# Optimization experiments

Hardware: AMD Instinct MI355X
Metric: run time of the kernel (lower is better)

The kernel has to match this reference:

```python
import jax, jax.numpy as jnp
import numpy as np

N_GAUSS = 512
PLANE = 512


def setup_inputs() -> dict:
    key = jax.random.key(0)
    k1, k2, k3, k4, k5 = jax.random.split(key, 5)
    mean = jax.random.uniform(k1, (N_GAUSS, 2, 1), dtype=jnp.float32)
    alpha = jax.random.uniform(k2, (N_GAUSS, 1), dtype=jnp.float32)
    scale = jax.random.uniform(k3, (N_GAUSS, 2), dtype=jnp.float32)
    theta = jax.random.uniform(k4, (N_GAUSS, 1), dtype=jnp.float32)
    rgb = jax.random.uniform(k5, (N_GAUSS, 3), dtype=jnp.float32)
    # render plane: torch.meshgrid(x, y, indexing='xy'), stack([x, y], -1)
    lin = jnp.linspace(0.0, 1.0, PLANE, dtype=jnp.float32)
    xx, yy = jnp.meshgrid(lin, lin, indexing='xy')
    pixels = jnp.stack([xx, yy], axis=-1)  # (H, W, 2)
    return {"mean": mean, "alpha": alpha, "scale": scale, "theta": theta,
            "rgb": rgb, "pixels": pixels}


def _forward(mean, alpha, scale, theta, rgb, pixels):
    two_pi = 2.0 * jnp.pi
    # covariance = R S S^T R^T with R from circular_activation(theta)
    ta = two_pi * theta                      # (N,1)
    c = jnp.cos(ta)
    s = jnp.sin(ta)
    rot = jnp.stack([jnp.concatenate([c, -s], axis=-1),
                     jnp.concatenate([s, c], axis=-1)], axis=-2)   # (N,2,2)
    smat = jnp.eye(2, dtype=scale.dtype)[None] * scale[..., None]  # (N,2,2)
    cov = rot @ smat @ jnp.swapaxes(smat, -1, -2) @ jnp.swapaxes(rot, -1, -2)
    a = cov[:, 0, 0]
    b01 = cov[:, 0, 1]
    b10 = cov[:, 1, 0]
    d = cov[:, 1, 1]
    det = a * d - b01 * b10                  # (N,)
    inv00 = d / det
    inv01 = -b01 / det
    inv10 = -b10 / det
    inv11 = a / det
    # quadratic form per pixel (analytic 2x2, same math as diff^T inv diff)
    mu = mean[:, :, 0]                       # (N,2)
    dx = pixels[None, :, :, 0] - mu[:, 0][:, None, None]  # (N,H,W)
    dy = pixels[None, :, :, 1] - mu[:, 1][:, None, None]  # (N,H,W)
    q = (inv00[:, None, None] * dx * dx
         + (inv01 + inv10)[:, None, None] * dx * dy
         + inv11[:, None, None] * dy * dy)
    prob = jnp.exp(-0.5 * q) / (two_pi * jnp.sqrt(det))[:, None, None]  # (N,H,W)
    splat = prob / jnp.max(prob)             # global max-normalize
    weighted = rgb * alpha                   # (N,3) rgb * alpha mask
    img = jnp.einsum('nhw,nc->hwc', splat, weighted)  # sum over gaussians
    return jax.nn.sigmoid(img)               # (H,W,3)


def reference(mean, alpha, scale, theta, rgb, pixels):
    return _forward(mean, alpha, scale, theta, rgb, pixels)
```

## Files before the change

### kernel.cpp

```cpp
#include <hip/hip_runtime.h>

#define NG 512
#define PLANE 512

typedef float v2f __attribute__((ext_vector_type(2)));

#define PRM_OFF  16
#define SLOT_OFF 4352

__global__ __launch_bounds__(256) void prep_kernel(
    const float* __restrict__ mean, const float* __restrict__ alpha,
    const float* __restrict__ scale, const float* __restrict__ theta,
    const float* __restrict__ rgb, float* __restrict__ ws) {
    const int n   = blockIdx.x;
    const int tid = threadIdx.x;

    const float TWO_PI = 6.283185307179586f;
    float th = theta[n];
    float c = __builtin_amdgcn_cosf(th);
    float s = __builtin_amdgcn_sinf(th);
    float sx = scale[2 * n], sy = scale[2 * n + 1];

    float m200 = (c * sx) * sx;
    float m201 = (-(s * sy)) * sy;
    float m210 = (s * sx) * sx;
    float m211 = (c * sy) * sy;
    float a   = m200 * c + m201 * (-s);
    float b01 = m200 * s + m201 * c;
    float b10 = m210 * c + m211 * (-s);
    float d   = m210 * s + m211 * c;

    float det = a * d - b01 * b10;
    float rdet = __builtin_amdgcn_rcpf(det);
    float inv00 = d * rdet;
    float inv01 = -b01 * rdet;
    float inv10 = -b10 * rdet;
    float inv11 = a * rdet;

    float norm = __builtin_amdgcn_rcpf(TWO_PI * __builtin_amdgcn_sqrtf(det));
    const float K = -0.5f * 1.4426950408889634f;

    float A_ = K * inv00;
    float B_ = K * (inv01 + inv10);
    float C_ = K * inv11;
    float mx = mean[2 * n], my = mean[2 * n + 1];
    float Lg = fmaf(-0.5f, __builtin_amdgcn_logf(det), -2.651496129472319f);

    if (tid == 0) {
        float w = alpha[n] * norm;
        float4* p = (float4*)(ws + PRM_OFF + 8 * n);
        p[0] = make_float4(A_, B_, C_, mx);
        p[1] = make_float4(my, w * rgb[3 * n], w * rgb[3 * n + 1], w * rgb[3 * n + 2]);
    }

    const float STEP = 1.0f / 511.0f;
    float inv2A = __builtin_amdgcn_rcpf(2.0f * A_);
    float t = -1e30f;
#pragma unroll
    for (int k = 0; k < 2; ++k) {
        int r = tid + (k << 8);
        float y  = (float)r * STEP;
        float dy = y - my;
        float bdy  = B_ * dy;
        float cdy2 = C_ * (dy * dy);
        float xstar = mx - bdy * inv2A;
        float xs = fminf(fmaxf(xstar, 0.0f), 1.0f);
        int i1 = min((int)(xs * 511.0f), 510);
#pragma unroll
        for (int kk = -1; kk <= 2; ++kk) {
            int i = max(0, min(i1 + kk, 511));
            float x = (float)i * STEP;
            float dx = x - mx;
            float q = fmaf(fmaf(A_, dx, bdy), dx, cdy2);
            t = fmaxf(t, q);
        }
    }
    t += Lg;

#pragma unroll
    for (int off = 32; off > 0; off >>= 1)
        t = fmaxf(t, __shfl_xor(t, off));
    __shared__ float sm[4];
    if ((tid & 63) == 0) sm[tid >> 6] = t;
    __syncthreads();
    if (tid == 0) {
        float mm = fmaxf(fmaxf(sm[0], sm[1]), fmaxf(sm[2], sm[3]));
        ws[SLOT_OFF + n] = mm;
    }
}

__global__ __launch_bounds__(512, 4) void splat_kernel(
    const float* __restrict__ pixels, const float* __restrict__ ws,
    float* __restrict__ out) {
    const int tid  = threadIdx.x;
    const int wv   = __builtin_amdgcn_readfirstlane(tid >> 6);
    const int lane = tid & 63;
    const int quad = blockIdx.x * 64 + lane;
    const int pbase = quad << 2;
    const int row  = blockIdx.x >> 1;

    __shared__ float4 shbuf[1536];

    {
        const float4* p = reinterpret_cast<const float4*>(ws + PRM_OFF) + 2 * tid;
        float4 p0 = p[0];
        float4 p1 = p[1];
        float yb = pixels[(row << 10) + 1];
        float dy   = yb - p1.x;
        float bdy  = p0.y * dy;
        float cdy2 = p0.z * (dy * dy);
        shbuf[2 * tid]     = make_float4(p0.x, p0.w, bdy, cdy2);
        shbuf[2 * tid + 1] = make_float4(p1.y, p1.z, p1.w, 0.f);
    }
    __syncthreads();

    float4 p01 = *reinterpret_cast<const float4*>(pixels + 2 * pbase);
    float4 p23 = *reinterpret_cast<const float4*>(pixels + 2 * pbase + 4);
    const v2f x01 = {p01.x, p01.z};
    const v2f x23 = {p23.x, p23.z};

    v2f ar01 = {0.f, 0.f}, ag01 = {0.f, 0.f}, ab01 = {0.f, 0.f};
    v2f ar23 = {0.f, 0.f}, ag23 = {0.f, 0.f}, ab23 = {0.f, 0.f};

    const float4* chunk = shbuf + (wv << 7);
#pragma unroll 8
    for (int n = 0; n < 64; ++n) {
        float4 ta = chunk[2 * n];
        float4 tb = chunk[2 * n + 1];

        float A_ = ta.x, mx = ta.y, bdy = ta.z, cdy2 = ta.w;
        v2f Av = {A_, A_}, mxv = {mx, mx}, bdyv = {bdy, bdy}, cdv = {cdy2, cdy2};

        v2f dx01 = x01 - mxv;
        v2f dx23 = x23 - mxv;
        v2f t01 = __builtin_elementwise_fma(Av, dx01, bdyv);
        v2f t23 = __builtin_elementwise_fma(Av, dx23, bdyv);
        v2f q01 = __builtin_elementwise_fma(t01, dx01, cdv);
        v2f q23 = __builtin_elementwise_fma(t23, dx23, cdv);

        v2f e01 = {__builtin_amdgcn_exp2f(q01.x), __builtin_amdgcn_exp2f(q01.y)};
        v2f e23 = {__builtin_amdgcn_exp2f(q23.x), __builtin_amdgcn_exp2f(q23.y)};

        v2f wrv = {tb.x, tb.x}, wgv = {tb.y, tb.y}, wbv = {tb.z, tb.z};
        ar01 = __builtin_elementwise_fma(e01, wrv, ar01);
        ag01 = __builtin_elementwise_fma(e01, wgv, ag01);
        ab01 = __builtin_elementwise_fma(e01, wbv, ab01);
        ar23 = __builtin_elementwise_fma(e23, wrv, ar23);
        ag23 = __builtin_elementwise_fma(e23, wgv, ag23);
        ab23 = __builtin_elementwise_fma(e23, wbv, ab23);
    }

    float invmax;
    {
        const float4* sl = reinterpret_cast<const float4*>(ws + SLOT_OFF) + 2 * lane;
        float4 s0 = sl[0], s1 = sl[1];
        float m = fmaxf(fmaxf(fmaxf(s0.x, s0.y), fmaxf(s0.z, s0.w)),
                        fmaxf(fmaxf(s1.x, s1.y), fmaxf(s1.z, s1.w)));
#pragma unroll
        for (int off = 32; off > 0; off >>= 1)
            m = fmaxf(m, __shfl_xor(m, off));
        invmax = __builtin_amdgcn_exp2f(-m);
    }

    __syncthreads();

    {
        const int base = ((wv << 6) + lane) * 3;
        shbuf[base + 0] = make_float4(ar01.x, ag01.x, ab01.x, ar01.y);
        shbuf[base + 1] = make_float4(ag01.y, ab01.y, ar23.x, ag23.x);
        shbuf[base + 2] = make_float4(ab23.x, ar23.y, ag23.y, ab23.y);
    }
    __syncthreads();

    if (tid < 192) {
        const int l    = tid / 3;
        const int slot = tid - 3 * l;
        float4 v = shbuf[l * 3 + slot];
#pragma unroll
        for (int cch = 1; cch < 8; ++cch) {
            float4 u = shbuf[((cch << 6) + l) * 3 + slot];
            v.x += u.x; v.y += u.y; v.z += u.z; v.w += u.w;
        }
        const float KE = 1.4426950408889634f;
#define SIG(x) __builtin_amdgcn_rcpf(1.0f + __builtin_amdgcn_exp2f(-KE * ((x) * invmax)))
        v.x = SIG(v.x); v.y = SIG(v.y); v.z = SIG(v.z); v.w = SIG(v.w);
#undef SIG
        reinterpret_cast<float4*>(out)[blockIdx.x * 192 + tid] = v;
    }
}

extern "C" void kernel_launch(void* const* d_in, const int* in_sizes, int n_in,
                              void* d_out, int out_size, void* d_ws, size_t ws_size,
                              hipStream_t stream) {
    const float* mean   = (const float*)d_in[0];
    const float* alpha  = (const float*)d_in[1];
    const float* scale  = (const float*)d_in[2];
    const float* theta  = (const float*)d_in[3];
    const float* rgb    = (const float*)d_in[4];
    const float* pixels = (const float*)d_in[5];
    float* out = (float*)d_out;
    float* ws  = (float*)d_ws;

    prep_kernel<<<512, 256, 0, stream>>>(mean, alpha, scale, theta, rgb, ws);

    splat_kernel<<<1024, 512, 0, stream>>>(pixels, ws, out);
}
```

Baseline: 91.04 us.

## Halve splat block size and expand quadratic form around pixel center

Shrinks the splat block from 512 to 256 threads, so each wave walks 128 Gaussians instead of 64 and the cross-wave reduction sums 4 partials instead of 8. The quadratic is re-expanded in u = x - 0.5 with precomputed beta/gamma coefficients and a per-pixel u^2, replacing the per-Gaussian subtract and two FMAs with two FMAs. This also packs the parameters more tightly in shared memory. Centering on 0.5 is meant to limit cancellation, but the expanded form can still differ slightly in precision.

New measurement: 101.2 us. 1.11x slower.

```diff
diff --git a/kernel.cpp b/kernel.cpp
--- a/kernel.cpp
+++ b/kernel.cpp
@@ -89,7 +89,7 @@
     }
 }
 
-__global__ __launch_bounds__(512, 4) void splat_kernel(
+__global__ __launch_bounds__(256, 8) void splat_kernel(
     const float* __restrict__ pixels, const float* __restrict__ ws,
     float* __restrict__ out) {
     const int tid  = threadIdx.x;
@@ -97,51 +97,58 @@
     const int lane = tid & 63;
     const int quad = blockIdx.x * 64 + lane;
     const int pbase = quad << 2;
-    const int row  = blockIdx.x >> 1;
-
-    __shared__ float4 shbuf[1536];
+    const int rrow = blockIdx.x >> 1;
+
+    __shared__ float4 shbuf[1024];
 
     {
-        const float4* p = reinterpret_cast<const float4*>(ws + PRM_OFF) + 2 * tid;
-        float4 p0 = p[0];
-        float4 p1 = p[1];
-        float yb = pixels[(row << 10) + 1];
-        float dy   = yb - p1.x;
-        float bdy  = p0.y * dy;
-        float cdy2 = p0.z * (dy * dy);
-        shbuf[2 * tid]     = make_float4(p0.x, p0.w, bdy, cdy2);
-        shbuf[2 * tid + 1] = make_float4(p1.y, p1.z, p1.w, 0.f);
+        float yb = pixels[(rrow << 10) + 1];
+#pragma unroll
+        for (int k = 0; k < 2; ++k) {
+            int g = tid + (k << 8);
+            const float4* p = reinterpret_cast<const float4*>(ws + PRM_OFF) + 2 * g;
+            float4 p0 = p[0];
+            float4 p1 = p[1];
+            float dy   = yb - p1.x;
+            float bdy  = p0.y * dy;
+            float cdy2 = p0.z * (dy * dy);
+            float mxp  = p0.w - 0.5f;
+            float beta  = fmaf(-2.0f * p0.x, mxp, bdy);
+            float gamma = fmaf(fmaf(p0.x, mxp, -bdy), mxp, cdy2);
+            shbuf[2 * g]     = make_float4(p0.x, beta, gamma, p1.y);
+            shbuf[2 * g + 1] = make_float4(p1.z, p1.w, 0.f, 0.f);
+        }
     }
     __syncthreads();
 
     float4 p01 = *reinterpret_cast<const float4*>(pixels + 2 * pbase);
     float4 p23 = *reinterpret_cast<const float4*>(pixels + 2 * pbase + 4);
-    const v2f x01 = {p01.x, p01.z};
-    const v2f x23 = {p23.x, p23.z};
+    const v2f half2 = {0.5f, 0.5f};
+    const v2f u01 = (v2f){p01.x, p01.z} - half2;
+    const v2f u23 = (v2f){p23.x, p23.z} - half2;
+    const v2f u01sq = u01 * u01;
+    const v2f u23sq = u23 * u23;
 
     v2f ar01 = {0.f, 0.f}, ag01 = {0.f, 0.f}, ab01 = {0.f, 0.f};
     v2f ar23 = {0.f, 0.f}, ag23 = {0.f, 0.f}, ab23 = {0.f, 0.f};
 
-    const float4* chunk = shbuf + (wv << 7);
+    const float4* chunk = shbuf + (wv << 8);
 #pragma unroll 8
-    for (int n = 0; n < 64; ++n) {
+    for (int n = 0; n < 128; ++n) {
         float4 ta = chunk[2 * n];
         float4 tb = chunk[2 * n + 1];
 
-        float A_ = ta.x, mx = ta.y, bdy = ta.z, cdy2 = ta.w;
-        v2f Av = {A_, A_}, mxv = {mx, mx}, bdyv = {bdy, bdy}, cdv = {cdy2, cdy2};
-
-        v2f dx01 = x01 - mxv;
-        v2f dx23 = x23 - mxv;
-        v2f t01 = __builtin_elementwise_fma(Av, dx01, bdyv);
-        v2f t23 = __builtin_elementwise_fma(Av, dx23, bdyv);
-        v2f q01 = __builtin_elementwise_fma(t01, dx01, cdv);
-        v2f q23 = __builtin_elementwise_fma(t23, dx23, cdv);
+        v2f Av = {ta.x, ta.x}, bev = {ta.y, ta.y}, gav = {ta.z, ta.z};
+
+        v2f q01 = __builtin_elementwise_fma(bev, u01,
+                    __builtin_elementwise_fma(Av, u01sq, gav));
+        v2f q23 = __builtin_elementwise_fma(bev, u23,
+                    __builtin_elementwise_fma(Av, u23sq, gav));
 
         v2f e01 = {__builtin_amdgcn_exp2f(q01.x), __builtin_amdgcn_exp2f(q01.y)};
         v2f e23 = {__builtin_amdgcn_exp2f(q23.x), __builtin_amdgcn_exp2f(q23.y)};
 
-        v2f wrv = {tb.x, tb.x}, wgv = {tb.y, tb.y}, wbv = {tb.z, tb.z};
+        v2f wrv = {ta.w, ta.w}, wgv = {tb.x, tb.x}, wbv = {tb.y, tb.y};
         ar01 = __builtin_elementwise_fma(e01, wrv, ar01);
         ag01 = __builtin_elementwise_fma(e01, wgv, ag01);
         ab01 = __builtin_elementwise_fma(e01, wbv, ab01);
@@ -177,7 +184,7 @@
         const int slot = tid - 3 * l;
         float4 v = shbuf[l * 3 + slot];
 #pragma unroll
-        for (int cch = 1; cch < 8; ++cch) {
+        for (int cch = 1; cch < 4; ++cch) {
             float4 u = shbuf[((cch << 6) + l) * 3 + slot];
             v.x += u.x; v.y += u.y; v.z += u.z; v.w += u.w;
         }
@@ -203,5 +210,5 @@
 
     prep_kernel<<<512, 256, 0, stream>>>(mean, alpha, scale, theta, rgb, ws);
 
-    splat_kernel<<<1024, 512, 0, stream>>>(pixels, ws, out);
+    splat_kernel<<<1024, 256, 0, stream>>>(pixels, ws, out);
 }
```
